# Optimization experiments

Hardware: AMD Instinct MI355X
Metric: run time of the kernel (lower is better)

The kernel has to match this reference:

```python
import jax, jax.numpy as jnp
import numpy as np

M, L, P, KK = 8, 3, 12, 9  # n_heads, n_levels, n_points, patch_size**2

def lrelu(v):
    return jnp.where(v >= 0, v, 0.1 * v)

def conv2d(x, w, b, pad):
    y = jax.lax.conv_general_dilated(x, w, (1, 1), [(pad, pad), (pad, pad)], dimension_numbers=('NCHW', 'OIHW', 'NCHW'))
    return y + b[None, :, None, None]

def trunk(x, w1, b1, w2, b2, w3, b3, w4, b4):
    h = lrelu(conv2d(x, w1, b1, 0))
    h = lrelu(conv2d(h, w2, b2, 1))
    h = lrelu(conv2d(h, w3, b3, 1))
    return conv2d(h, w4, b4, 0)

def grid_sample(img, gx, gy, align_corners):
    # img [N,C,H,W]; gx,gy [N,Q] normalized to [-1,1]; bilinear, zeros padding
    N, C, H, W = img.shape
    if align_corners:
        ix = (gx + 1.0) * 0.5 * (W - 1)
        iy = (gy + 1.0) * 0.5 * (H - 1)
    else:
        ix = ((gx + 1.0) * W - 1.0) * 0.5
        iy = ((gy + 1.0) * H - 1.0) * 0.5
    ix0 = jnp.floor(ix); iy0 = jnp.floor(iy)
    wx1 = ix - ix0; wy1 = iy - iy0
    flat = img.reshape(N, C, H * W)
    def gather(xi, yi, wgt):
        valid = (xi >= 0) & (xi <= W - 1) & (yi >= 0) & (yi <= H - 1)
        idx = (jnp.clip(yi, 0, H - 1) * W + jnp.clip(xi, 0, W - 1)).astype(jnp.int32)
        v = jnp.take_along_axis(flat, idx[:, None, :], axis=2)
        return v * (wgt * valid)[:, None, :]
    return (gather(ix0, iy0, (1 - wx1) * (1 - wy1)) + gather(ix0 + 1, iy0, wx1 * (1 - wy1))
            + gather(ix0, iy0 + 1, (1 - wx1) * wy1) + gather(ix0 + 1, iy0 + 1, wx1 * wy1))

def flow_warp(img, flow):
    # img [n,c,h,w]; flow [n,2,h,w] in pixels; torch grid_sample align_corners=True, zeros padding
    n, c, h, w = img.shape
    gy, gx = jnp.meshgrid(jnp.arange(h, dtype=img.dtype), jnp.arange(w, dtype=img.dtype), indexing='ij')
    gxn = 2.0 * (gx[None] + flow[:, 0]) / max(w - 1, 1) - 1.0
    gyn = 2.0 * (gy[None] + flow[:, 1]) / max(h - 1, 1) - 1.0
    return grid_sample(img, gxn.reshape(n, -1), gyn.reshape(n, -1), True).reshape(n, c, h, w)

def msdeform_attn(value, loc, attn, h, w):
    # pytorch MSDeformAttn core: value [N,L*HW,M,D]; loc [N,HW,M,L,Pt,2]; attn [N,HW,M,L,Pt]
    N, _, _, D = value.shape
    HW = h * w
    Pt = loc.shape[4]
    grids = 2.0 * loc - 1.0
    sampled = []
    for l in range(L):
        v = value[:, l * HW:(l + 1) * HW].transpose(0, 2, 3, 1).reshape(N * M, D, h, w)
        g = grids[:, :, :, l].transpose(0, 2, 1, 3, 4).reshape(N * M, HW * Pt, 2)
        s = grid_sample(v, g[..., 0], g[..., 1], False)  # [N*M, D, HW*Pt]
        sampled.append(s.reshape(N * M, D, HW, Pt))
    sampled = jnp.concatenate(sampled, axis=-1)  # [N*M, D, HW, L*Pt]
    aw = attn.transpose(0, 2, 1, 3, 4).reshape(N * M, HW, L * Pt)
    out = jnp.einsum('ndqp,nqp->nqd', sampled, aw)
    return out.reshape(N, M, HW, D).transpose(0, 2, 1, 3).reshape(N, HW, M * D)

def _forward(x, flow_1, flow_2, flip_flow_1, flip_flow_2, aw_w1, aw_b1, aw_w2, aw_b2, aw_w3, aw_b3, aw_w4, aw_b4, so_w1, so_b1, so_w2, so_b2, so_w3, so_b3, so_w4, so_b4, po_w1, po_b1, po_w2, po_b2, po_w3, po_b3, po_w4, po_b4, vp_w, vp_b, op_w1, op_b1, op_w2, op_b2):
    n, t, c, h, w = x.shape
    HW = h * w
    flow_cn1 = flow_1
    flow_cn2 = flow_1 + flow_warp(flow_2, flow_cn1)
    warp1 = flow_warp(x[:, 1], flow_cn1)
    warp2 = flow_warp(x[:, 2], flow_cn2)
    extra = jnp.concatenate([x[:, 0], warp1, warp2, flow_cn1, flow_cn2], axis=1)  # [n, 3c+4, h, w]
    value = conv2d(x.reshape(n, t * c, h, w), vp_w, vp_b, 0)
    off = trunk(extra, so_w1, so_b1, so_w2, so_b2, so_w3, so_b3, so_w4, so_b4)
    aw = trunk(extra, aw_w1, aw_b1, aw_w2, aw_b2, aw_w3, aw_b3, aw_w4, aw_b4)
    po = trunk(extra, po_w1, po_b1, po_w2, po_b2, po_w3, po_b3, po_w4, po_b4)
    value = value.reshape(n, t, c, HW).transpose(0, 1, 3, 2).reshape(n, t * HW, M, c // M)
    off = off.reshape(n, -1, HW).transpose(0, 2, 1).reshape(n, HW, M, L, P, 2)
    po = po.reshape(n, -1, HW).transpose(0, 2, 1).reshape(n, HW, M, L, P)
    po = jax.nn.sigmoid(po) * 3.0
    aw = aw.reshape(n, -1, HW).transpose(0, 2, 1).reshape(n, HW, M, L * P * KK)
    aw = jax.nn.softmax(aw, axis=-1).reshape(n, HW, M, L, P * KK)
    # flow-guided per-level offsets: level0 zeros, level1 flow_cn1, level2 flow_cn2
    f1 = flow_cn1.reshape(n, 2, HW).transpose(0, 2, 1)
    f2 = flow_cn2.reshape(n, 2, HW).transpose(0, 2, 1)
    fstack = jnp.stack([jnp.zeros_like(f1), f1, f2], axis=2)  # [n,HW,L,2]
    off = off + fstack[:, :, None, :, None, :]
    # 3x3 patch around each sampling point, scaled by learned patch offsets
    a = jnp.arange(-1, 2, dtype=x.dtype)
    pnx, pny = jnp.meshgrid(a, a, indexing='ij')
    p_n = jnp.stack([pnx, pny], axis=-1).reshape(KK, 2)
    off = off[..., None, :] + p_n * po[..., None, None]  # [n,HW,M,L,P,KK,2]
    off = off.reshape(n, HW, M, L, P * KK, 2)
    # reference points (valid ratios == 1)
    ry = (jnp.arange(h, dtype=x.dtype) + 0.5) / h
    rx = (jnp.arange(w, dtype=x.dtype) + 0.5) / w
    gy, gx = jnp.meshgrid(ry, rx, indexing='ij')
    ref = jnp.stack([gx, gy], axis=-1).reshape(1, HW, 1, 1, 1, 2)
    norm = jnp.array([w, h], dtype=x.dtype)
    loc = ref + off / norm
    out = msdeform_attn(value, loc, aw, h, w)  # [n, HW, c]
    feat = out.reshape(n, h, w, c).transpose(0, 3, 1, 2)
    res = conv2d(lrelu(conv2d(feat, op_w1, op_b1, 0)), op_w2, op_b2, 0)
    return res + x[:, 0]

def setup_inputs():
    key = jax.random.key(0)
    keys = jax.random.split(key, 64)
    it = iter(range(64))
    def nrm(shape, scale):
        return jax.random.normal(keys[next(it)], shape, jnp.float32) * scale
    n, t, c, h, w = 1, 3, 64, 64, 64
    Cin = t * c + 4  # 196
    d = {}
    d['x'] = nrm((n, t, c, h, w), 1.0)
    for nm in ['flow_1', 'flow_2', 'flip_flow_1', 'flip_flow_2']:
        d[nm] = nrm((n, 2, h, w), 1.5)
    def branch(prefix, out_ch, final_scale):
        d[prefix + '_w1'] = nrm((64, Cin, 1, 1), 1.0 / np.sqrt(Cin))
        d[prefix + '_b1'] = nrm((64,), 0.01)
        d[prefix + '_w2'] = nrm((64, 64, 3, 3), 1.0 / np.sqrt(64 * 9))
        d[prefix + '_b2'] = nrm((64,), 0.01)
        d[prefix + '_w3'] = nrm((64, 64, 3, 3), 1.0 / np.sqrt(64 * 9))
        d[prefix + '_b3'] = nrm((64,), 0.01)
        d[prefix + '_w4'] = nrm((out_ch, 64, 1, 1), final_scale)
        d[prefix + '_b4'] = nrm((out_ch,), 0.01)
    branch('aw', M * L * P * KK, 0.01)
    branch('so', M * L * P * 2, 0.01)
    branch('po', M * L * P, 0.01)
    d['vp_w'] = nrm((t * c, t * c, 1, 1), 1.0 / np.sqrt(t * c))
    d['vp_b'] = nrm((t * c,), 0.01)
    d['op_w1'] = nrm((c, c, 1, 1), 1.0 / np.sqrt(c))
    d['op_b1'] = nrm((c,), 0.01)
    d['op_w2'] = nrm((c, c, 1, 1), 1.0 / np.sqrt(c))
    d['op_b2'] = nrm((c,), 0.01)
    return d

def reference(x, flow_1, flow_2, flip_flow_1, flip_flow_2, aw_w1, aw_b1, aw_w2, aw_b2, aw_w3, aw_b3, aw_w4, aw_b4, so_w1, so_b1, so_w2, so_b2, so_w3, so_b3, so_w4, so_b4, po_w1, po_b1, po_w2, po_b2, po_w3, po_b3, po_w4, po_b4, vp_w, vp_b, op_w1, op_b1, op_w2, op_b2):
    return _forward(x, flow_1, flow_2, flip_flow_1, flip_flow_2, aw_w1, aw_b1, aw_w2, aw_b2, aw_w3, aw_b3, aw_w4, aw_b4, so_w1, so_b1, so_w2, so_b2, so_w3, so_b3, so_w4, so_b4, po_w1, po_b1, po_w2, po_b2, po_w3, po_b3, po_w4, po_b4, vp_w, vp_b, op_w1, op_b1, op_w2, op_b2)
```

## Files before the change

kernel.cpp:

```cpp
#include <hip/hip_runtime.h>
#include <hip/hip_bf16.h>
#include <math.h>

#define HWN 4096
#define VROW 72
#define VYP 36
#define VSZ_B (24 * VYP * VROW * 16)

typedef __attribute__((ext_vector_type(8))) short short8;
typedef __attribute__((ext_vector_type(4))) float f32x4;
typedef __attribute__((ext_vector_type(2))) float f32x2;

__device__ __forceinline__ float lrelu_f(float v) { return v >= 0.f ? v : 0.1f * v; }

__device__ __forceinline__ unsigned short f2bf(float f) {
  union { float f; unsigned u; } v; v.f = f;
  unsigned r = v.u + 0x7fff + ((v.u >> 16) & 1);
  return (unsigned short)(r >> 16);
}
__device__ __forceinline__ float bf2f(unsigned short u) {
  union { unsigned u; float f; } v; v.u = ((unsigned)u) << 16; return v.f;
}
__device__ __forceinline__ float bf_lo(unsigned u) {
  union { unsigned u; float f; } v; v.u = u << 16; return v.f;
}
__device__ __forceinline__ float bf_hi(unsigned u) {
  union { unsigned u; float f; } v; v.u = u & 0xffff0000u; return v.f;
}
template <bool HI>
__device__ __forceinline__ f32x2 cvt8(unsigned u) {
  return __builtin_amdgcn_cvt_pk_f32_fp8((int)u, HI);
}

__device__ __forceinline__ float bilin_zero(const float* __restrict__ img, float ix, float iy) {
  float fx0 = floorf(ix), fy0 = floorf(iy);
  int x0 = (int)fx0, y0 = (int)fy0;
  float wx1 = ix - fx0, wy1 = iy - fy0;
  float wx0 = 1.f - wx1, wy0 = 1.f - wy1;
  float acc = 0.f;
  if ((unsigned)y0 < 64u) {
    if ((unsigned)x0 < 64u)       acc += wx0 * wy0 * img[y0 * 64 + x0];
    if ((unsigned)(x0 + 1) < 64u) acc += wx1 * wy0 * img[y0 * 64 + x0 + 1];
  }
  if ((unsigned)(y0 + 1) < 64u) {
    if ((unsigned)x0 < 64u)       acc += wx0 * wy1 * img[(y0 + 1) * 64 + x0];
    if ((unsigned)(x0 + 1) < 64u) acc += wx1 * wy1 * img[(y0 + 1) * 64 + x0 + 1];
  }
  return acc;
}

__global__ void k_pre(
    const float* __restrict__ x, const float* __restrict__ flow1, const float* __restrict__ flow2,
    const float* so_w4, const float* po_w4, const float* aw_w4,
    const float* so_b4, const float* po_b4, const float* aw_b4,
    const float* so_b1, const float* po_b1, const float* aw_b1,
    const float* so_b2, const float* po_b2, const float* aw_b2,
    const float* so_b3, const float* po_b3, const float* aw_b3,
    const float* so_w1, const float* po_w1, const float* aw_w1,
    const float* so_w2, const float* po_w2, const float* aw_w2,
    const float* so_w3, const float* po_w3, const float* aw_w3,
    const float* op_w1, const float* op_w2, const float* vp_w,
    unsigned short* Wtail, float* btail, float* b1c, float* b2c, float* b3c,
    unsigned short* o1b, unsigned short* o2b, unsigned short* W1,
    unsigned short* W2g, unsigned short* W3g, unsigned short* vpb,
    unsigned short* xb, float* fcn2, unsigned char* v8) {
  __shared__ unsigned short tile[64 * 65];
  __shared__ unsigned short wrow[576];
  int gx = blockIdx.x;
  int tid = threadIdx.x;
  if (gx < 864) {
    int t = gx * 256 + tid;
    int row = t >> 6, k = t & 63;
    float v = row < 576 ? so_w4[row * 64 + k]
            : row < 864 ? po_w4[(row - 576) * 64 + k]
                        : aw_w4[(row - 864) * 64 + k];
    Wtail[t] = f2bf(v);
  } else if (gx < 912) {
    int t = (gx - 864) * 256 + tid;
    if (t < 3456) {
      btail[t] = t < 576 ? so_b4[t] : t < 864 ? po_b4[t - 576] : aw_b4[t - 864];
    } else if (t < 3648) {
      int i = t - 3456; b1c[i] = i < 64 ? so_b1[i] : i < 128 ? po_b1[i - 64] : aw_b1[i - 128];
    } else if (t < 3840) {
      int i = t - 3648; b2c[i] = i < 64 ? so_b2[i] : i < 128 ? po_b2[i - 64] : aw_b2[i - 128];
    } else if (t < 4032) {
      int i = t - 3840; b3c[i] = i < 64 ? so_b3[i] : i < 128 ? po_b3[i - 64] : aw_b3[i - 128];
    } else if (t < 8128) {
      o1b[t - 4032] = f2bf(op_w1[t - 4032]);
    } else if (t < 12224) {
      o2b[t - 8128] = f2bf(op_w2[t - 8128]);
    }
  } else if (gx < 1080) {
    int t = (gx - 912) * 256 + tid;
    if (t < 192 * 224) {
      int row = t / 224, k = t % 224;
      int tr = row >> 6, lco = row & 63;
      const float* s = tr == 0 ? so_w1 : tr == 1 ? po_w1 : aw_w1;
      W1[t] = (k < 196) ? f2bf(s[lco * 196 + k]) : (unsigned short)0;
    }
  } else if (gx < 1464) {
    int b = gx - 1080;
    int which = b >= 192;
    b &= 191;
    int tr = b >> 6, co = b & 63;
    const float* s;
    if (!which) s = tr == 0 ? so_w2 : tr == 1 ? po_w2 : aw_w2;
    else        s = tr == 0 ? so_w3 : tr == 1 ? po_w3 : aw_w3;
    unsigned short* d = which ? W3g : W2g;
#pragma unroll
    for (int j = tid; j < 576; j += 256) wrow[j] = f2bf(s[co * 576 + j]);
    __syncthreads();
#pragma unroll
    for (int j = tid; j < 576; j += 256)
      d[((size_t)tr * 64 + co) * 576 + j] = wrow[(j & 63) * 9 + (j >> 6)];
  } else if (gx < 1608) {
    int t = (gx - 1464) * 256 + tid;
    if (t < 192 * 192) vpb[t] = f2bf(vp_w[t]);
  } else if (gx < 1800) {
    int b = gx - 1608;
    int ptile = b & 63, cg = b >> 6;
    int px = tid & 63, ch0 = (tid >> 6) * 16;
#pragma unroll
    for (int i = 0; i < 16; i++) {
      float v = x[(size_t)(cg * 64 + ch0 + i) * HWN + ptile * 64 + px];
      tile[(ch0 + i) * 65 + px] = f2bf(v);
    }
    __syncthreads();
    int c = tid & 63, pl0 = (tid >> 6) * 16;
#pragma unroll
    for (int i = 0; i < 16; i++)
      xb[(size_t)(ptile * 64 + pl0 + i) * 192 + cg * 64 + c] = tile[c * 65 + pl0 + i];
  } else if (gx < 1816) {
    int p = (gx - 1800) * 256 + tid;
    int px = p & 63, py = p >> 6;
    float fx = flow1[p], fy = flow1[HWN + p];
    float ix = (float)px + fx, iy = (float)py + fy;
    fcn2[p] = fx + bilin_zero(flow2, ix, iy);
    fcn2[HWN + p] = fy + bilin_zero(flow2 + HWN, ix, iy);
  } else {
    int i = (gx - 1816) * 256 + tid;
    if (i < 2 * VSZ_B / 16) ((uint4*)v8)[i] = make_uint4(0, 0, 0, 0);
  }
}

__global__ void k_extra(const unsigned short* __restrict__ xb, const float* __restrict__ flow1,
                        const float* __restrict__ fcn2, unsigned short* __restrict__ extra) {
  int w = threadIdx.x >> 6, c = threadIdx.x & 63;
  int p = blockIdx.x * 4 + w;
  int px = p & 63, py = p >> 6;
  float fx1 = flow1[p], fy1 = flow1[HWN + p];
  float fx2 = fcn2[p],  fy2 = fcn2[HWN + p];
  extra[(size_t)p * 224 + c] = xb[(size_t)p * 192 + c];
#pragma unroll
  for (int lev = 0; lev < 2; lev++) {
    float ix = (float)px + (lev ? fx2 : fx1);
    float iy = (float)py + (lev ? fy2 : fy1);
    float fx0 = floorf(ix), fy0 = floorf(iy);
    int x0 = (int)fx0, y0 = (int)fy0;
    float wx1 = ix - fx0, wy1 = iy - fy0;
    float wx0 = 1.f - wx1, wy0 = 1.f - wy1;
    int coff = (lev + 1) * 64;
    float acc = 0.f;
    if ((unsigned)y0 < 64u) {
      if ((unsigned)x0 < 64u)       acc += wx0 * wy0 * bf2f(xb[(size_t)(y0 * 64 + x0) * 192 + coff + c]);
      if ((unsigned)(x0 + 1) < 64u) acc += wx1 * wy0 * bf2f(xb[(size_t)(y0 * 64 + x0 + 1) * 192 + coff + c]);
    }
    if ((unsigned)(y0 + 1) < 64u) {
      if ((unsigned)x0 < 64u)       acc += wx0 * wy1 * bf2f(xb[(size_t)((y0 + 1) * 64 + x0) * 192 + coff + c]);
      if ((unsigned)(x0 + 1) < 64u) acc += wx1 * wy1 * bf2f(xb[(size_t)((y0 + 1) * 64 + x0 + 1) * 192 + coff + c]);
    }
    extra[(size_t)p * 224 + coff + c] = f2bf(acc);
  }
  if (c < 2) {
    extra[(size_t)p * 224 + 192 + c] = f2bf(flow1[c * HWN + p]);
    extra[(size_t)p * 224 + 194 + c] = f2bf(fcn2[c * HWN + p]);
  }
  if (c < 28) extra[(size_t)p * 224 + 196 + c] = 0;
}

__global__ __launch_bounds__(128) void k_gemm2(
    const unsigned short* __restrict__ A0, const unsigned short* __restrict__ Wm0,
    const float* __restrict__ bias0, unsigned short* __restrict__ out0,
    const unsigned short* __restrict__ A1, const unsigned short* __restrict__ Wm1,
    const float* __restrict__ bias1, unsigned short* __restrict__ out1) {
  int z = blockIdx.z;
  const unsigned short* A = z ? A1 : A0;
  const unsigned short* Wm = z ? Wm1 : Wm0;
  const float* bias = z ? bias1 : bias0;
  unsigned short* out = z ? out1 : out0;
  int K = z ? 224 : 192;

  int wv = threadIdx.x >> 6;
  int l = threadIdx.x & 63;
  int lm = l & 15, lq = l >> 4;
  int p0 = blockIdx.x * 32 + wv * 16;
  int co0 = blockIdx.y * 32;

  f32x4 acc[2];
#pragma unroll
  for (int nt = 0; nt < 2; nt++) {
    float bv = bias[co0 + nt * 16 + lm];
    acc[nt] = (f32x4){bv, bv, bv, bv};
  }
  const unsigned short* ap = A + (size_t)(p0 + lm) * K + lq * 8;
  const unsigned short* wp = Wm + (size_t)(co0 + lm) * K + lq * 8;
  for (int k0 = 0; k0 < K; k0 += 32) {
    short8 af = *(const short8*)(ap + k0);
#pragma unroll
    for (int nt = 0; nt < 2; nt++) {
      short8 bf = *(const short8*)(wp + (size_t)nt * 16 * K + k0);
      acc[nt] = __builtin_amdgcn_mfma_f32_16x16x32_bf16(af, bf, acc[nt], 0, 0, 0);
    }
  }
#pragma unroll
  for (int nt = 0; nt < 2; nt++) {
    int co = co0 + nt * 16 + lm;
#pragma unroll
    for (int r = 0; r < 4; r++) {
      int p = p0 + lq * 4 + r;
      float v = acc[nt][r];
      if (z) v = lrelu_f(v);
      out[(size_t)p * 192 + co] = f2bf(v);
    }
  }
}

__global__ __launch_bounds__(128) void k_conv3g(const unsigned short* __restrict__ h,
                                                const unsigned short* __restrict__ Wm,
                                                const float* __restrict__ bias,
                                                unsigned short* __restrict__ out) {
  int wv = threadIdx.x >> 6;
  int l = threadIdx.x & 63;
  int lm = l & 15, lq = l >> 4;
  int p0 = blockIdx.x * 32 + wv * 16;
  int co0 = blockIdx.y * 16;
  int t = blockIdx.z;
  int p = p0 + lm;
  int px = p & 63, py = p >> 6;

  float bv = bias[t * 64 + co0 + lm];
  f32x4 acc = (f32x4){bv, bv, bv, bv};
  const unsigned short* wp = Wm + ((size_t)t * 64 + co0 + lm) * 576 + lq * 8;
#pragma unroll
  for (int kidx = 0; kidx < 9; kidx++) {
    int ky = kidx / 3, kx = kidx % 3;
    int pp = p + (ky - 1) * 64 + (kx - 1);
    bool valid = ((unsigned)(px + kx - 1) < 64u) && ((unsigned)(py + ky - 1) < 64u);
    const unsigned short* apb = h + (size_t)pp * 192 + t * 64 + lq * 8;
#pragma unroll
    for (int c2 = 0; c2 < 2; c2++) {
      short8 af = {};
      if (valid) af = *(const short8*)(apb + c2 * 32);
      short8 bf = *(const short8*)(wp + kidx * 64 + c2 * 32);
      acc = __builtin_amdgcn_mfma_f32_16x16x32_bf16(af, bf, acc, 0, 0, 0);
    }
  }
#pragma unroll
  for (int r = 0; r < 4; r++) {
    int po_ = p0 + lq * 4 + r;
    out[(size_t)po_ * 192 + t * 64 + co0 + lm] = f2bf(lrelu_f(acc[r]));
  }
}

__global__ __launch_bounds__(256) void k_tail(const unsigned short* __restrict__ A,
                                              const unsigned short* __restrict__ Wm,
                                              const float* __restrict__ bias,
                                              unsigned short* __restrict__ out,
                                              const unsigned short* __restrict__ vsb,
                                              unsigned char* __restrict__ v8) {
  if (blockIdx.y >= 108) {
    int i = ((blockIdx.y - 108) * 64 + blockIdx.x) * 256 + threadIdx.x;
    int lm = i % 24, p = i / 24;
    uint4 vv = ((const uint4*)vsb)[p * 24 + lm];
    int lo = 0, hi = 0;
    lo = __builtin_amdgcn_cvt_pk_fp8_f32(bf_lo(vv.x), bf_hi(vv.x), lo, false);
    lo = __builtin_amdgcn_cvt_pk_fp8_f32(bf_lo(vv.y), bf_hi(vv.y), lo, true);
    hi = __builtin_amdgcn_cvt_pk_fp8_f32(bf_lo(vv.z), bf_hi(vv.z), hi, false);
    hi = __builtin_amdgcn_cvt_pk_fp8_f32(bf_lo(vv.w), bf_hi(vv.w), hi, true);
    uint2 pk; pk.x = (unsigned)lo; pk.y = (unsigned)hi;
    int y = p >> 6, xx = p & 63;
    int ypA = (y >> 1) + 1, slotA = y & 1;
    int ypB = (y + 1) >> 1, slotB = (y & 1) ^ 1;
    *(uint2*)(v8 + (((lm * VYP + ypA) * VROW + xx + 2) * 16 + slotA * 8)) = pk;
    *(uint2*)(v8 + VSZ_B + (((lm * VYP + ypB) * VROW + xx + 2) * 16 + slotB * 8)) = pk;
    return;
  }
  int wv = threadIdx.x >> 6;
  int l = threadIdx.x & 63;
  int lm = l & 15, lq = l >> 4;
  int p0 = blockIdx.x * 64 + wv * 16;
  int co0 = blockIdx.y * 32;
  int t = (co0 < 576) ? 0 : (co0 < 864 ? 1 : 2);

  f32x4 acc[2];
#pragma unroll
  for (int nt = 0; nt < 2; nt++) {
    float bv = bias[co0 + nt * 16 + lm];
    acc[nt] = (f32x4){bv, bv, bv, bv};
  }
  const unsigned short* ap = A + (size_t)(p0 + lm) * 192 + t * 64 + lq * 8;
  const unsigned short* wp = Wm + (size_t)(co0 + lm) * 64 + lq * 8;
#pragma unroll
  for (int k0 = 0; k0 < 64; k0 += 32) {
    short8 af = *(const short8*)(ap + k0);
#pragma unroll
    for (int nt = 0; nt < 2; nt++) {
      short8 bf = *(const short8*)(wp + (size_t)nt * 16 * 64 + k0);
      acc[nt] = __builtin_amdgcn_mfma_f32_16x16x32_bf16(af, bf, acc[nt], 0, 0, 0);
    }
  }
#pragma unroll
  for (int nt = 0; nt < 2; nt++) {
    int co = co0 + nt * 16 + lm;
#pragma unroll
    for (int r = 0; r < 4; r++) {
      int p = p0 + lq * 4 + r;
      float v = acc[nt][r];
      if (t == 2) v = __expf(v);
      else if (t == 1) v = 3.f * __builtin_amdgcn_rcpf(1.f + __expf(-v));
      out[(size_t)p * 3456 + co] = f2bf(v);
    }
  }
}

__global__ __launch_bounds__(256, 4) void k_msdout(
    const unsigned char* __restrict__ v8,
    const unsigned short* __restrict__ to,
    const float* __restrict__ flow1, const float* __restrict__ fcn2,
    const unsigned short* __restrict__ o1b, const float* __restrict__ bias1,
    const unsigned short* __restrict__ o2b, const float* __restrict__ bias2,
    const float* __restrict__ x, float* __restrict__ out) {
  __shared__ float featL[2][64];
  __shared__ float hopL[2][64];
  int tid = threadIdx.x;
  int yl = tid & 15;
  int m = (tid >> 4) & 7;
  int pl = tid >> 7;
  int p = blockIdx.x * 2 + pl;
  int px = p & 63, py = p >> 6;

  float fx1 = flow1[p], fy1 = flow1[HWN + p];
  float fx2 = fcn2[p],  fy2 = fcn2[HWN + p];

  const unsigned short* row = to + (size_t)p * 3456;

  f32x2 accv[4];
#pragma unroll
  for (int d = 0; d < 4; d++) accv[d] = (f32x2){0.f, 0.f};
  float wsum = 0.f;

#pragma unroll 1
  for (int pair = yl; pair < 36; pair += 16) {
    int lv = pair / 12, pt = pair % 12;
    float fx = (lv == 1) ? fx1 : ((lv == 2) ? fx2 : 0.f);
    float fy = (lv == 1) ? fy1 : ((lv == 2) ? fy2 : 0.f);
    int ch = (m * 3 + lv) * 12 + pt;
    unsigned ow = *(const unsigned*)(row + ch * 2);
    float ox = bf_lo(ow);
    float oy = bf_hi(ow);
    float s = bf2f(row[576 + ch]);
    float bx = (float)px + ox + fx;
    float by = (float)py + oy + fy;
    int lmoff = (lv * 8 + m) * (VYP * VROW * 16);
    const unsigned short* lgp = row + 864 + m * 324 + lv * 108 + pt * 9;

    const unsigned char* rb[3];
    float yw0[3], yw1[3];
#pragma unroll
    for (int j = 0; j < 3; j++) {
      float cy = by + (float)(j - 1) * s;
      float fy0 = floorf(cy);
      yw1[j] = cy - fy0; yw0[j] = 1.f - yw1[j];
      int y0 = min(max((int)fy0, -2), 66);
      int par = y0 & 1;
      int yp = (y0 + 2 - par) >> 1;
      rb[j] = v8 + par * VSZ_B + lmoff + yp * (VROW * 16);
    }
#pragma unroll 1
    for (int jx = 0; jx < 3; jx++) {
      float cx = bx + (float)(jx - 1) * s;
      float fx0 = floorf(cx);
      float wx1 = cx - fx0, wx0 = 1.f - wx1;
      int xoff = (min(max((int)fx0, -2), 66) + 2) * 16;
      const unsigned short* lg3 = lgp + jx * 3;
#pragma unroll
      for (int jy = 0; jy < 3; jy++) {
        float wgt = bf2f(lg3[jy]);
        wsum += wgt;
        const unsigned char* vb = rb[jy] + xoff;
        uint4 qa = *(const uint4*)vb;
        uint4 qb = *(const uint4*)(vb + 16);

        float w00 = wgt * wx0 * yw0[jy], w01 = wgt * wx0 * yw1[jy];
        float w10 = wgt * wx1 * yw0[jy], w11 = wgt * wx1 * yw1[jy];
        f32x2 W00 = (f32x2){w00, w00}, W01 = (f32x2){w01, w01};
        f32x2 W10 = (f32x2){w10, w10}, W11 = (f32x2){w11, w11};

        accv[0] += W00 * cvt8<false>(qa.x) + W01 * cvt8<false>(qa.z)
                 + W10 * cvt8<false>(qb.x) + W11 * cvt8<false>(qb.z);
        accv[1] += W00 * cvt8<true>(qa.x)  + W01 * cvt8<true>(qa.z)
                 + W10 * cvt8<true>(qb.x)  + W11 * cvt8<true>(qb.z);
        accv[2] += W00 * cvt8<false>(qa.y) + W01 * cvt8<false>(qa.w)
                 + W10 * cvt8<false>(qb.y) + W11 * cvt8<false>(qb.w);
        accv[3] += W00 * cvt8<true>(qa.y)  + W01 * cvt8<true>(qa.w)
                 + W10 * cvt8<true>(qb.y)  + W11 * cvt8<true>(qb.w);
      }
    }
  }
#pragma unroll
  for (int mask = 1; mask < 16; mask <<= 1) {
    wsum += __shfl_xor(wsum, mask);
#pragma unroll
    for (int d = 0; d < 4; d++) {
      accv[d].x += __shfl_xor(accv[d].x, mask);
      accv[d].y += __shfl_xor(accv[d].y, mask);
    }
  }
  if (yl < 8) {
    float inv = __builtin_amdgcn_rcpf(wsum);
    float r = 0.f;
#pragma unroll
    for (int d = 0; d < 8; d++) {
      float v = (d & 1) ? accv[d >> 1].y : accv[d >> 1].x;
      r = (d == yl) ? v : r;
    }
    featL[pl][m * 8 + yl] = r * inv;
  }
  __syncthreads();

  if (tid < 128) {
    int ql = tid >> 6, co = tid & 63;
    float a = bias1[co];
    const uint4* wr = (const uint4*)(o1b + co * 64);
#pragma unroll
    for (int c8 = 0; c8 < 8; c8++) {
      uint4 wv = wr[c8];
      int ci = c8 * 8;
      a += bf_lo(wv.x) * featL[ql][ci]     + bf_hi(wv.x) * featL[ql][ci + 1]
         + bf_lo(wv.y) * featL[ql][ci + 2] + bf_hi(wv.y) * featL[ql][ci + 3]
         + bf_lo(wv.z) * featL[ql][ci + 4] + bf_hi(wv.z) * featL[ql][ci + 5]
         + bf_lo(wv.w) * featL[ql][ci + 6] + bf_hi(wv.w) * featL[ql][ci + 7];
    }
    hopL[ql][co] = lrelu_f(a);
  }
  __syncthreads();

  if (tid < 128) {
    int ql = tid >> 6, co = tid & 63;
    int p2 = blockIdx.x * 2 + ql;
    float a = bias2[co];
    const uint4* wr = (const uint4*)(o2b + co * 64);
#pragma unroll
    for (int c8 = 0; c8 < 8; c8++) {
      uint4 wv = wr[c8];
      int ci = c8 * 8;
      a += bf_lo(wv.x) * hopL[ql][ci]     + bf_hi(wv.x) * hopL[ql][ci + 1]
         + bf_lo(wv.y) * hopL[ql][ci + 2] + bf_hi(wv.y) * hopL[ql][ci + 3]
         + bf_lo(wv.z) * hopL[ql][ci + 4] + bf_hi(wv.z) * hopL[ql][ci + 5]
         + bf_lo(wv.w) * hopL[ql][ci + 6] + bf_hi(wv.w) * hopL[ql][ci + 7];
    }
    out[(size_t)co * HWN + p2] = a + x[(size_t)co * HWN + p2];
  }
}

extern "C" void kernel_launch(void* const* d_in, const int* in_sizes, int n_in,
                              void* d_out, int out_size, void* d_ws, size_t ws_size,
                              hipStream_t stream) {
  const float* x     = (const float*)d_in[0];
  const float* flow1 = (const float*)d_in[1];
  const float* flow2 = (const float*)d_in[2];
  const float* aw_w1 = (const float*)d_in[5];
  const float* aw_b1 = (const float*)d_in[6];
  const float* aw_w2 = (const float*)d_in[7];
  const float* aw_b2 = (const float*)d_in[8];
  const float* aw_w3 = (const float*)d_in[9];
  const float* aw_b3 = (const float*)d_in[10];
  const float* aw_w4 = (const float*)d_in[11];
  const float* aw_b4 = (const float*)d_in[12];
  const float* so_w1 = (const float*)d_in[13];
  const float* so_b1 = (const float*)d_in[14];
  const float* so_w2 = (const float*)d_in[15];
  const float* so_b2 = (const float*)d_in[16];
  const float* so_w3 = (const float*)d_in[17];
  const float* so_b3 = (const float*)d_in[18];
  const float* so_w4 = (const float*)d_in[19];
  const float* so_b4 = (const float*)d_in[20];
  const float* po_w1 = (const float*)d_in[21];
  const float* po_b1 = (const float*)d_in[22];
  const float* po_w2 = (const float*)d_in[23];
  const float* po_b2 = (const float*)d_in[24];
  const float* po_w3 = (const float*)d_in[25];
  const float* po_b3 = (const float*)d_in[26];
  const float* po_w4 = (const float*)d_in[27];
  const float* po_b4 = (const float*)d_in[28];
  const float* vp_w  = (const float*)d_in[29];
  const float* vp_b  = (const float*)d_in[30];
  const float* op_w1 = (const float*)d_in[31];
  const float* op_b1 = (const float*)d_in[32];
  const float* op_w2 = (const float*)d_in[33];
  const float* op_b2 = (const float*)d_in[34];

  char* base = (char*)d_ws;
  size_t off = 0;
  auto alloc = [&](size_t bytes) { void* pp = base + off; off = (off + bytes + 255) & ~(size_t)255; return pp; };

  float* fcn2  = (float*)alloc(2 * HWN * 4);
  unsigned short* xb    = (unsigned short*)alloc(192 * HWN * 2);
  unsigned short* vsb   = (unsigned short*)alloc(192 * HWN * 2);
  unsigned short* extra = (unsigned short*)alloc(224 * HWN * 2);
  unsigned short* h1    = (unsigned short*)alloc(192 * HWN * 2);
  unsigned short* h2    = (unsigned short*)alloc(192 * HWN * 2);
  unsigned short* h3    = (unsigned short*)alloc(192 * HWN * 2);
  unsigned short* to    = (unsigned short*)alloc((size_t)3456 * HWN * 2);
  unsigned char* v8     = (unsigned char*)alloc((size_t)VSZ_B * 2);
  unsigned short* Wtail = (unsigned short*)alloc(3456 * 64 * 2);
  float* btail = (float*)alloc(3456 * 4);
  float* b1c   = (float*)alloc(192 * 4);
  float* b2c   = (float*)alloc(192 * 4);
  float* b3c   = (float*)alloc(192 * 4);
  unsigned short* o1b = (unsigned short*)alloc(64 * 64 * 2);
  unsigned short* o2b = (unsigned short*)alloc(64 * 64 * 2);
  unsigned short* W1  = (unsigned short*)alloc(192 * 224 * 2);
  unsigned short* W2g = (unsigned short*)alloc(3 * 64 * 576 * 2);
  unsigned short* W3g = (unsigned short*)alloc(3 * 64 * 576 * 2);
  unsigned short* vpb = (unsigned short*)alloc(192 * 192 * 2);

  k_pre<<<2302, 256, 0, stream>>>(
      x, flow1, flow2,
      so_w4, po_w4, aw_w4, so_b4, po_b4, aw_b4,
      so_b1, po_b1, aw_b1, so_b2, po_b2, aw_b2, so_b3, po_b3, aw_b3,
      so_w1, po_w1, aw_w1, so_w2, po_w2, aw_w2, so_w3, po_w3, aw_w3,
      op_w1, op_w2, vp_w,
      Wtail, btail, b1c, b2c, b3c, o1b, o2b, W1, W2g, W3g, vpb, xb, fcn2, v8);

  k_extra<<<1024, 256, 0, stream>>>(xb, flow1, fcn2, extra);

  k_gemm2<<<dim3(128, 6, 2), 128, 0, stream>>>(xb, vpb, vp_b, vsb, extra, W1, b1c, h1);

  k_conv3g<<<dim3(128, 4, 3), 128, 0, stream>>>(h1, W2g, b2c, h2);
  k_conv3g<<<dim3(128, 4, 3), 128, 0, stream>>>(h2, W3g, b3c, h3);
  k_tail<<<dim3(64, 114), 256, 0, stream>>>(h3, Wtail, btail, to, vsb, v8);

  k_msdout<<<2048, 256, 0, stream>>>(v8, to, flow1, fcn2, o1b, op_b1, o2b, op_b2, x, (float*)d_out);
}
```

Measured before the change: 222.4 us.

## Fuse third conv with tail 1x1 projection via LDS; move fp8 value pack into conv2

The second 3x3 grouped conv and the tail 1x1 projection become one kernel: each 128-thread block computes h3 for 16 pixels into shared memory, then loops over all 3456 output channels. This removes the h3 global round trip and one launch. The fp8 repacking of the projected value tensor moves from the tail kernel into extra blocks of the first conv launch. The fused kernel runs only 256 blocks with long serial loops, so occupancy and latency hiding drop sharply compared with the previous wide grids.

```diff
diff --git a/kernel.cpp b/kernel.cpp
--- a/kernel.cpp
+++ b/kernel.cpp
@@ -228,7 +228,32 @@
 __global__ __launch_bounds__(128) void k_conv3g(const unsigned short* __restrict__ h,
                                                 const unsigned short* __restrict__ Wm,
                                                 const float* __restrict__ bias,
-                                                unsigned short* __restrict__ out) {
+                                                unsigned short* __restrict__ out,
+                                                const unsigned short* __restrict__ vsb,
+                                                unsigned char* __restrict__ v8) {
+  if (blockIdx.z == 3) {
+    int b = blockIdx.y * 128 + blockIdx.x;
+    int i = b * 128 + threadIdx.x;
+#pragma unroll
+    for (int rep = 0; rep < 2; rep++, i += 65536) {
+      if (i < 98304) {
+        int lm = i % 24, p = i / 24;
+        uint4 vv = ((const uint4*)vsb)[p * 24 + lm];
+        int lo = 0, hi = 0;
+        lo = __builtin_amdgcn_cvt_pk_fp8_f32(bf_lo(vv.x), bf_hi(vv.x), lo, false);
+        lo = __builtin_amdgcn_cvt_pk_fp8_f32(bf_lo(vv.y), bf_hi(vv.y), lo, true);
+        hi = __builtin_amdgcn_cvt_pk_fp8_f32(bf_lo(vv.z), bf_hi(vv.z), hi, false);
+        hi = __builtin_amdgcn_cvt_pk_fp8_f32(bf_lo(vv.w), bf_hi(vv.w), hi, true);
+        uint2 pk; pk.x = (unsigned)lo; pk.y = (unsigned)hi;
+        int y = p >> 6, xx = p & 63;
+        int ypA = (y >> 1) + 1, slotA = y & 1;
+        int ypB = (y + 1) >> 1, slotB = (y & 1) ^ 1;
+        *(uint2*)(v8 + (((lm * VYP + ypA) * VROW + xx + 2) * 16 + slotA * 8)) = pk;
+        *(uint2*)(v8 + VSZ_B + (((lm * VYP + ypB) * VROW + xx + 2) * 16 + slotB * 8)) = pk;
+      }
+    }
+    return;
+  }
   int wv = threadIdx.x >> 6;
   int l = threadIdx.x & 63;
   int lm = l & 15, lq = l >> 4;
@@ -262,63 +287,80 @@
   }
 }
 
-__global__ __launch_bounds__(256) void k_tail(const unsigned short* __restrict__ A,
-                                              const unsigned short* __restrict__ Wm,
-                                              const float* __restrict__ bias,
-                                              unsigned short* __restrict__ out,
-                                              const unsigned short* __restrict__ vsb,
-                                              unsigned char* __restrict__ v8) {
-  if (blockIdx.y >= 108) {
-    int i = ((blockIdx.y - 108) * 64 + blockIdx.x) * 256 + threadIdx.x;
-    int lm = i % 24, p = i / 24;
-    uint4 vv = ((const uint4*)vsb)[p * 24 + lm];
-    int lo = 0, hi = 0;
-    lo = __builtin_amdgcn_cvt_pk_fp8_f32(bf_lo(vv.x), bf_hi(vv.x), lo, false);
-    lo = __builtin_amdgcn_cvt_pk_fp8_f32(bf_lo(vv.y), bf_hi(vv.y), lo, true);
-    hi = __builtin_amdgcn_cvt_pk_fp8_f32(bf_lo(vv.z), bf_hi(vv.z), hi, false);
-    hi = __builtin_amdgcn_cvt_pk_fp8_f32(bf_lo(vv.w), bf_hi(vv.w), hi, true);
-    uint2 pk; pk.x = (unsigned)lo; pk.y = (unsigned)hi;
-    int y = p >> 6, xx = p & 63;
-    int ypA = (y >> 1) + 1, slotA = y & 1;
-    int ypB = (y + 1) >> 1, slotB = (y & 1) ^ 1;
-    *(uint2*)(v8 + (((lm * VYP + ypA) * VROW + xx + 2) * 16 + slotA * 8)) = pk;
-    *(uint2*)(v8 + VSZ_B + (((lm * VYP + ypB) * VROW + xx + 2) * 16 + slotB * 8)) = pk;
-    return;
-  }
-  int wv = threadIdx.x >> 6;
-  int l = threadIdx.x & 63;
+__global__ __launch_bounds__(128) void k_c3tail(const unsigned short* __restrict__ h2,
+                                                const unsigned short* __restrict__ W3g,
+                                                const float* __restrict__ b3c,
+                                                const unsigned short* __restrict__ Wtail,
+                                                const float* __restrict__ btail,
+                                                unsigned short* __restrict__ to) {
+  __shared__ unsigned short h3L[16 * 200];
+  int tid = threadIdx.x;
+  int wv = tid >> 6;
+  int l = tid & 63;
   int lm = l & 15, lq = l >> 4;
-  int p0 = blockIdx.x * 64 + wv * 16;
-  int co0 = blockIdx.y * 32;
-  int t = (co0 < 576) ? 0 : (co0 < 864 ? 1 : 2);
-
-  f32x4 acc[2];
-#pragma unroll
-  for (int nt = 0; nt < 2; nt++) {
-    float bv = bias[co0 + nt * 16 + lm];
-    acc[nt] = (f32x4){bv, bv, bv, bv};
-  }
-  const unsigned short* ap = A + (size_t)(p0 + lm) * 192 + t * 64 + lq * 8;
-  const unsigned short* wp = Wm + (size_t)(co0 + lm) * 64 + lq * 8;
-#pragma unroll
-  for (int k0 = 0; k0 < 64; k0 += 32) {
-    short8 af = *(const short8*)(ap + k0);
+  int p0 = blockIdx.x * 16;
+  int p = p0 + lm;
+  int px = p & 63, py = p >> 6;
+
+#pragma unroll 1
+  for (int ct = 0; ct < 6; ct++) {
+    int gco = wv * 96 + ct * 16;
+    int t = gco >> 6;
+    float bv = b3c[gco + lm];
+    f32x4 acc = (f32x4){bv, bv, bv, bv};
+    const unsigned short* wp = W3g + (size_t)(gco + lm) * 576 + lq * 8;
+#pragma unroll
+    for (int kidx = 0; kidx < 9; kidx++) {
+      int ky = kidx / 3, kx = kidx % 3;
+      int pp = p + (ky - 1) * 64 + (kx - 1);
+      bool valid = ((unsigned)(px + kx - 1) < 64u) && ((unsigned)(py + ky - 1) < 64u);
+      const unsigned short* apb = h2 + (size_t)pp * 192 + t * 64 + lq * 8;
+#pragma unroll
+      for (int c2 = 0; c2 < 2; c2++) {
+        short8 af = {};
+        if (valid) af = *(const short8*)(apb + c2 * 32);
+        short8 bf = *(const short8*)(wp + kidx * 64 + c2 * 32);
+        acc = __builtin_amdgcn_mfma_f32_16x16x32_bf16(af, bf, acc, 0, 0, 0);
+      }
+    }
+#pragma unroll
+    for (int r = 0; r < 4; r++)
+      h3L[(lq * 4 + r) * 200 + gco + lm] = f2bf(lrelu_f(acc[r]));
+  }
+  __syncthreads();
+
+#pragma unroll 1
+  for (int ti = 0; ti < 54; ti++) {
+    int co0 = wv * 1728 + ti * 32;
+    int t = (co0 < 576) ? 0 : (co0 < 864 ? 1 : 2);
+    f32x4 acc[2];
 #pragma unroll
     for (int nt = 0; nt < 2; nt++) {
-      short8 bf = *(const short8*)(wp + (size_t)nt * 16 * 64 + k0);
-      acc[nt] = __builtin_amdgcn_mfma_f32_16x16x32_bf16(af, bf, acc[nt], 0, 0, 0);
-    }
-  }
-#pragma unroll
-  for (int nt = 0; nt < 2; nt++) {
-    int co = co0 + nt * 16 + lm;
-#pragma unroll
-    for (int r = 0; r < 4; r++) {
-      int p = p0 + lq * 4 + r;
-      float v = acc[nt][r];
-      if (t == 2) v = __expf(v);
-      else if (t == 1) v = 3.f * __builtin_amdgcn_rcpf(1.f + __expf(-v));
-      out[(size_t)p * 3456 + co] = f2bf(v);
+      float bv = btail[co0 + nt * 16 + lm];
+      acc[nt] = (f32x4){bv, bv, bv, bv};
+    }
+    const unsigned short* ap = h3L + lm * 200 + t * 64 + lq * 8;
+    const unsigned short* wp = Wtail + (size_t)(co0 + lm) * 64 + lq * 8;
+#pragma unroll
+    for (int k0 = 0; k0 < 64; k0 += 32) {
+      short8 af = *(const short8*)(ap + k0);
+#pragma unroll
+      for (int nt = 0; nt < 2; nt++) {
+        short8 bf = *(const short8*)(wp + (size_t)nt * 16 * 64 + k0);
+        acc[nt] = __builtin_amdgcn_mfma_f32_16x16x32_bf16(af, bf, acc[nt], 0, 0, 0);
+      }
+    }
+#pragma unroll
+    for (int nt = 0; nt < 2; nt++) {
+      int co = co0 + nt * 16 + lm;
+#pragma unroll
+      for (int r = 0; r < 4; r++) {
+        int pw = p0 + lq * 4 + r;
+        float v = acc[nt][r];
+        if (t == 2) v = __expf(v);
+        else if (t == 1) v = 3.f * __builtin_amdgcn_rcpf(1.f + __expf(-v));
+        to[(size_t)pw * 3456 + co] = f2bf(v);
+      }
     }
   }
 }
@@ -510,7 +552,6 @@
   unsigned short* extra = (unsigned short*)alloc(224 * HWN * 2);
   unsigned short* h1    = (unsigned short*)alloc(192 * HWN * 2);
   unsigned short* h2    = (unsigned short*)alloc(192 * HWN * 2);
-  unsigned short* h3    = (unsigned short*)alloc(192 * HWN * 2);
   unsigned short* to    = (unsigned short*)alloc((size_t)3456 * HWN * 2);
   unsigned char* v8     = (unsigned char*)alloc((size_t)VSZ_B * 2);
   unsigned short* Wtail = (unsigned short*)alloc(3456 * 64 * 2);
@@ -537,9 +578,9 @@
 
   k_gemm2<<<dim3(128, 6, 2), 128, 0, stream>>>(xb, vpb, vp_b, vsb, extra, W1, b1c, h1);
 
-  k_conv3g<<<dim3(128, 4, 3), 128, 0, stream>>>(h1, W2g, b2c, h2);
-  k_conv3g<<<dim3(128, 4, 3), 128, 0, stream>>>(h2, W3g, b3c, h3);
-  k_tail<<<dim3(64, 114), 256, 0, stream>>>(h3, Wtail, btail, to, vsb, v8);
+  k_conv3g<<<dim3(128, 4, 4), 128, 0, stream>>>(h1, W2g, b2c, h2, vsb, v8);
+
+  k_c3tail<<<256, 128, 0, stream>>>(h2, W3g, b3c, Wtail, btail, to);
 
   k_msdout<<<2048, 256, 0, stream>>>(v8, to, flow1, fcn2, o1b, op_b1, o2b, op_b2, x, (float*)d_out);
 }
```

Result: slower. 256.9 us (+15.5%).
